# Performance work log

Measured on AMD Instinct MI355X. Metric: run time of the kernel, lower is better.

The kernel has to match this reference:

```python
import jax, jax.numpy as jnp
import numpy as np
from jax import lax

VOCAB, EMB, HID, SEQ, BATCH = 50000, 512, 256, 64, 128


def _lstm_dir(x, Wih, Whh, bih, bhh):
    # x: (L,B,E); Wih: (4H,E); Whh: (4H,H); torch gate order i,f,g,o
    B = x.shape[1]
    H = Whh.shape[1]
    xg = jnp.einsum('lbe,ge->lbg', x, Wih) + (bih + bhh)  # precompute input contribution

    def step(carry, g_in):
        h, c = carry
        g = g_in + h @ Whh.T
        i, f, gg, o = jnp.split(g, 4, axis=-1)
        c = jax.nn.sigmoid(f) * c + jax.nn.sigmoid(i) * jnp.tanh(gg)
        h = jax.nn.sigmoid(o) * jnp.tanh(c)
        return (h, c), h

    z = jnp.zeros((B, H), x.dtype)
    _, hs = lax.scan(step, (z, z), xg)
    return hs  # (L,B,H)


def _bilstm(x, Wih_f, Whh_f, bih_f, bhh_f, Wih_b, Whh_b, bih_b, bhh_b):
    hf = _lstm_dir(x, Wih_f, Whh_f, bih_f, bhh_f)
    hb = _lstm_dir(x[::-1], Wih_b, Whh_b, bih_b, bhh_b)[::-1]
    return jnp.concatenate([hf, hb], axis=-1)  # (L,B,2H)


def _forward(tokens1, tokens2, emb, Wih_f, Whh_f, bih_f, bhh_f, Wih_b, Whh_b, bih_b, bhh_b):
    L, B = tokens1.shape
    w = (Wih_f, Whh_f, bih_f, bhh_f, Wih_b, Whh_b, bih_b, bhh_b)
    # original applies self.lstm_1 to BOTH sentences (lstm_2 unused)
    o1 = _bilstm(emb[tokens1], *w)  # (L,B,D)
    o2 = _bilstm(emb[tokens2], *w)
    D = o1.shape[-1]
    mp1 = o1.max(axis=0)  # adaptive_max_pool1d over time -> (B,D)
    # torch .view on contiguous (L,B,D): raw reshape, replicated faithfully
    att = jnp.einsum('bd,bdl->bl', mp1, o2.reshape(B, D, L))
    att_sm = jax.nn.softmax(att, axis=1)  # per-row softmax over L
    new_pool = jnp.einsum('bl,bld->bd', att_sm, o2.reshape(B, L, D))
    # commonWords: d[i] = LAST index j in sen1 with sen1[j]==sen2[i], else -1
    s1, s2 = tokens1.T, tokens2.T  # (B,L)
    match = s2[:, :, None] == s1[:, None, :]  # (B,L2,L1)
    d = jnp.max(jnp.where(match, jnp.arange(L)[None, None, :], -1), axis=2)  # (B,L)
    mask = (d > 1) & (s2 > 0)  # note strict > 1 as in original
    pos = jnp.clip(d, 0, L - 1)
    o1b = jnp.transpose(o1, (1, 0, 2))  # (B,L,D)
    gath1 = jnp.take_along_axis(o1b, pos[:, :, None], axis=1)  # outputs_1[d[i], b]
    neg = jnp.finfo(o1.dtype).min
    has = jnp.any(mask, axis=1)[:, None]
    e1h = jnp.where(has, jnp.max(jnp.where(mask[:, :, None], gath1, neg), axis=1), 0.0)
    o2b = jnp.transpose(o2, (1, 0, 2))
    e2h = jnp.where(has, jnp.max(jnp.where(mask[:, :, None], o2b, neg), axis=1), 0.0)
    sim = jnp.exp(-jnp.sum(jnp.abs(mp1 - new_pool), axis=1))
    return sim, e1h, e2h


def setup_inputs() -> dict:
    key = jax.random.key(0)
    ks = jax.random.split(key, 8)
    H4 = 4 * HID

    def w(k, shape, fan):
        return (jax.random.normal(k, shape, jnp.float32) / np.float32(np.sqrt(fan))).astype(jnp.float32)

    return {
        'tokens1': jax.random.randint(ks[0], (SEQ, BATCH), 0, VOCAB),
        'tokens2': jax.random.randint(ks[1], (SEQ, BATCH), 0, VOCAB),
        'emb': jax.random.normal(ks[2], (VOCAB, EMB), jnp.float32) * 0.1,
        'Wih_f': w(ks[3], (H4, EMB), EMB),
        'Whh_f': w(ks[4], (H4, HID), HID),
        'bih_f': jnp.full((H4,), 0.01, jnp.float32),
        'bhh_f': jnp.full((H4,), 0.01, jnp.float32),
        'Wih_b': w(ks[5], (H4, EMB), EMB),
        'Whh_b': w(ks[6], (H4, HID), HID),
        'bih_b': jnp.full((H4,), 0.01, jnp.float32),
        'bhh_b': jnp.full((H4,), 0.01, jnp.float32),
    }


def reference(tokens1, tokens2, emb, Wih_f, Whh_f, bih_f, bhh_f, Wih_b, Whh_b, bih_b, bhh_b):
    return _forward(tokens1, tokens2, emb, Wih_f, Whh_f, bih_f, bhh_f, Wih_b, Whh_b, bih_b, bhh_b)
```

## Files before the change

kernel.cpp:

```cpp
#include <hip/hip_runtime.h>
#include <hip/hip_bf16.h>
#include <math.h>

#define L_SEQ 64
#define NB    128
#define EMBD  512
#define HID   256
#define G4    1024
#define NCOL  2048
#define DDIM  512
#define MS    (L_SEQ*NB)
#define MTOT  (2*MS)

typedef __bf16 bf16_t;
typedef bf16_t bf16x4 __attribute__((ext_vector_type(4)));
typedef bf16_t bf16x8 __attribute__((ext_vector_type(8)));
typedef float  floatx4 __attribute__((ext_vector_type(4)));
typedef float  floatx8 __attribute__((ext_vector_type(8)));

__device__ __forceinline__ bf16x8 cvt_bf16x8(floatx8 v) {
    bf16x8 r;
    r[0]=(bf16_t)v[0]; r[1]=(bf16_t)v[1]; r[2]=(bf16_t)v[2]; r[3]=(bf16_t)v[3];
    r[4]=(bf16_t)v[4]; r[5]=(bf16_t)v[5]; r[6]=(bf16_t)v[6]; r[7]=(bf16_t)v[7];
    return r;
}

__device__ __forceinline__ void gload_lds16(const bf16_t* g, bf16_t* l) {
    __builtin_amdgcn_global_load_lds(
        (const __attribute__((address_space(1))) unsigned int*)(g),
        (__attribute__((address_space(3))) unsigned int*)(l), 16, 0, 0);
}

__device__ __forceinline__ float fsigmoid(float x) {
    return __builtin_amdgcn_rcpf(1.0f + __expf(-x));
}
__device__ __forceinline__ float ftanh(float x) {
    return 1.0f - 2.0f * __builtin_amdgcn_rcpf(__expf(2.0f*x) + 1.0f);
}

#define LDS_BARRIER() asm volatile("s_waitcnt lgkmcnt(0)\n\ts_barrier" ::: "memory")

__global__ __launch_bounds__(256) void k_pack_a(const int* __restrict__ t1,
                                                const int* __restrict__ t2,
                                                const float* __restrict__ emb,
                                                bf16_t* __restrict__ A)
{
    int gid = blockIdx.x*256 + threadIdx.x;
    int row = gid >> 6;
    int k8  = (gid & 63) * 8;
    int tok = (row < MS) ? t1[row] : t2[row - MS];
    floatx8 v = *(const floatx8*)(emb + (size_t)tok*EMBD + k8);
    *(bf16x8*)(A + (size_t)row*EMBD + k8) = cvt_bf16x8(v);
}

__global__ __launch_bounds__(256) void k_pack_b(const float* __restrict__ wih_f,
                                                const float* __restrict__ wih_b,
                                                bf16_t* __restrict__ B)
{
    int gid = blockIdx.x*256 + threadIdx.x;
    int n   = gid >> 6;
    int k8  = (gid & 63) * 8;
    const float* src = (n >= 1024) ? (wih_b + (size_t)(n-1024)*EMBD)
                                   : (wih_f + (size_t)n*EMBD);
    *(bf16x8*)(B + (size_t)n*EMBD + k8) = cvt_bf16x8(*(const floatx8*)(src + k8));
}

__global__ __launch_bounds__(256) void k_pack_whh(const float* __restrict__ whh_f,
                                                  const float* __restrict__ whh_b,
                                                  bf16_t* __restrict__ whhB)
{
    int gid = blockIdx.x*256 + threadIdx.x;
    int r2  = gid >> 5;
    int k8  = (gid & 31) * 8;
    const float* src = (r2 >= 1024) ? (whh_b + (size_t)(r2-1024)*HID)
                                    : (whh_f + (size_t)r2*HID);
    *(bf16x8*)(whhB + (size_t)r2*HID + k8) = cvt_bf16x8(*(const floatx8*)(src + k8));
}

__global__ __launch_bounds__(256) void k_pack_bias(const float* __restrict__ bih_f,
                                                   const float* __restrict__ bhh_f,
                                                   const float* __restrict__ bih_b,
                                                   const float* __restrict__ bhh_b,
                                                   float* __restrict__ bias)
{
    int n = blockIdx.x*256 + threadIdx.x;
    bias[n] = (n >= 1024) ? (bih_b[n-1024] + bhh_b[n-1024])
                          : (bih_f[n] + bhh_f[n]);
}

__global__ __launch_bounds__(256) void xg_gemm4(const bf16_t* __restrict__ A,
                                                const bf16_t* __restrict__ B,
                                                const float* __restrict__ bias,
                                                bf16_t* __restrict__ xgT)
{
    __shared__ bf16_t As[128*32];
    __shared__ bf16_t Bs[128*32];
    const int tid  = threadIdx.x;
    const int wid  = tid >> 6;
    const int lane = tid & 63;
    const int l15  = lane & 15;
    const int quad = lane >> 4;
    const int m0   = blockIdx.y * 128;
    const int n0   = blockIdx.x * 128;
    const int mw   = (wid & 1) * 64;
    const int nw   = (wid >> 1) * 64;

    float biasv[4];
#pragma unroll
    for (int ni = 0; ni < 4; ++ni) biasv[ni] = bias[n0 + nw + ni*16 + l15];

    const int srow = tid >> 2;
    const int sk8  = (tid & 3) * 8;

    floatx4 acc[4][4] = {};
    for (int kk = 0; kk < EMBD; kk += 32) {
#pragma unroll
        for (int inst = 0; inst < 2; ++inst) {
            gload_lds16(A + (size_t)(m0 + inst*64 + srow)*EMBD + kk + sk8,
                        As + inst*2048 + wid*512);
            gload_lds16(B + (size_t)(n0 + inst*64 + srow)*EMBD + kk + sk8,
                        Bs + inst*2048 + wid*512);
        }
        __syncthreads();
        bf16x8 a[4], b[4];
#pragma unroll
        for (int mi = 0; mi < 4; ++mi)
            a[mi] = *(const bf16x8*)(As + (mw + mi*16 + l15)*32 + quad*8);
#pragma unroll
        for (int ni = 0; ni < 4; ++ni)
            b[ni] = *(const bf16x8*)(Bs + (nw + ni*16 + l15)*32 + quad*8);
#pragma unroll
        for (int mi = 0; mi < 4; ++mi)
#pragma unroll
            for (int ni = 0; ni < 4; ++ni)
                acc[mi][ni] = __builtin_amdgcn_mfma_f32_16x16x32_bf16(
                                  a[mi], b[ni], acc[mi][ni], 0, 0, 0);
        __syncthreads();
    }

    const int sent = blockIdx.y >> 6;
    const int l    = blockIdx.y & 63;
    const int dir  = n0 >> 10;
    const int s2   = sent*2 + dir;
#pragma unroll
    for (int mi = 0; mi < 4; ++mi)
#pragma unroll
        for (int ni = 0; ni < 4; ++ni) {
            int gcol = (n0 & 1023) + nw + ni*16 + l15;
            int b    = mw + mi*16 + quad*4;
            int ch   = b >> 4;
            int bi   = b & 15;
            bf16x4 v;
#pragma unroll
            for (int r = 0; r < 4; ++r) v[r] = (bf16_t)(acc[mi][ni][r] + biasv[ni]);
            *(bf16x4*)(xgT + ((size_t)((s2*8 + ch)*64 + l)*1024 + gcol)*16 + bi) = v;
        }
}

__global__
__attribute__((amdgpu_flat_work_group_size(1024, 1024), amdgpu_waves_per_eu(4, 4)))
void lstm_scan8(
    const bf16_t* __restrict__ whhB,
    const bf16_t* __restrict__ xgT,
    float* __restrict__ o1, float* __restrict__ o2)
{
    extern __shared__ char smem[];
    bf16_t* hb = (bf16_t*)smem;
    bf16_t* BL = (bf16_t*)(smem + 16384);

    const int tid  = threadIdx.x;
    const int wv   = tid >> 6;
    const int lane = tid & 63;
    const int l15  = lane & 15;
    const int quad = lane >> 4;
    const int s2   = blockIdx.y;
    const int sent = s2 >> 1;
    const int dr   = s2 & 1;
    const int chunk= blockIdx.x;
    const int b0   = chunk * 16;
    float* o = sent ? o2 : o1;
    const bf16_t* bb = whhB + (size_t)dr * (1024*HID);


#pragma unroll
    for (int g = 0; g < 4; ++g) {
        const int col = g*256 + wv*16 + l15;
#pragma unroll
        for (int ksl = 0; ksl < 2; ++ksl)
            gload_lds16(bb + (size_t)col*HID + (4+ksl)*32 + quad*8,
                        BL + (size_t)((wv*4 + g)*2 + ksl)*512);
    }

    bf16x8 bwc[4][4];
#pragma unroll
    for (int g = 0; g < 4; ++g) {
        const bf16_t* cp = bb + (size_t)(g*256 + wv*16 + l15)*HID + quad*8;
#pragma unroll
        for (int ks = 0; ks < 4; ++ks)
            bwc[g][ks] = *(const volatile bf16x8*)(cp + ks*32);
    }

    for (int i = tid; i < 4096; i += 1024) hb[i] = (bf16_t)0.0f;
    __syncthreads();

    float cst[4] = {};
    int pp = 0;

    for (int t = 0; t < L_SEQ; ++t) {
        const int lt = dr ? (L_SEQ-1-t) : t;
        asm volatile("" ::: "memory");

        bf16x4 xvc[4];
        {
            const bf16_t* xp = xgT + (size_t)((s2*8 + chunk)*64 + lt)*16384;
#pragma unroll
            for (int g = 0; g < 4; ++g)
                xvc[g] = *(const bf16x4*)(xp + (size_t)(g*256 + wv*16 + l15)*16
                                          + quad*4);
        }

        floatx4 acc[4] = {};
        if (t > 0) {
            bf16x8 sb[4];
#pragma unroll
            for (int g = 0; g < 4; ++g) {
                const bf16_t* cp = bb + (size_t)(g*256 + wv*16 + l15)*HID;
                sb[g] = *(const bf16x8*)(cp + 6*32 + quad*8);
            }

            const bf16_t* fr = hb + pp*4096;
#pragma unroll
            for (int ks = 0; ks < 4; ++ks) {
                bf16x8 af = *(const bf16x8*)(fr + ((ks*4 + quad)*16 + l15)*8);
#pragma unroll
                for (int g = 0; g < 4; ++g)
                    acc[g] = __builtin_amdgcn_mfma_f32_16x16x32_bf16(
                                 af, bwc[g][ks], acc[g], 0, 0, 0);
            }
            {
                bf16x8 af6 = *(const bf16x8*)(fr + ((6*4 + quad)*16 + l15)*8);
#pragma unroll
                for (int g = 0; g < 4; ++g)
                    acc[g] = __builtin_amdgcn_mfma_f32_16x16x32_bf16(
                                 af6, sb[g], acc[g], 0, 0, 0);
            }
#pragma unroll
            for (int g = 0; g < 4; ++g) {
                const bf16_t* cp = bb + (size_t)(g*256 + wv*16 + l15)*HID;
                sb[g] = *(const bf16x8*)(cp + 7*32 + quad*8);
            }
#pragma unroll
            for (int ksl = 0; ksl < 2; ++ksl) {
                bf16x8 af = *(const bf16x8*)(fr + (((4+ksl)*4 + quad)*16 + l15)*8);
#pragma unroll
                for (int g = 0; g < 4; ++g) {
                    bf16x8 bl = *(const bf16x8*)(BL + (size_t)((wv*4 + g)*2 + ksl)*512
                                                 + lane*8);
                    acc[g] = __builtin_amdgcn_mfma_f32_16x16x32_bf16(
                                 af, bl, acc[g], 0, 0, 0);
                }
            }
            {
                bf16x8 af7 = *(const bf16x8*)(fr + ((7*4 + quad)*16 + l15)*8);
#pragma unroll
                for (int g = 0; g < 4; ++g)
                    acc[g] = __builtin_amdgcn_mfma_f32_16x16x32_bf16(
                                 af7, sb[g], acc[g], 0, 0, 0);
            }
        }

        bf16_t* fw = hb + (pp^1)*4096;
        const int j = wv*16 + l15;
        float* orow = o + (size_t)(lt*NB + b0)*DDIM + dr*HID + j;
#pragma unroll
        for (int r = 0; r < 4; ++r) {
            const int m = quad*4 + r;
            float gi = acc[0][r] + (float)xvc[0][r];
            float gf = acc[1][r] + (float)xvc[1][r];
            float gg = acc[2][r] + (float)xvc[2][r];
            float go = acc[3][r] + (float)xvc[3][r];
            float cv = fsigmoid(gf)*cst[r] + fsigmoid(gi)*ftanh(gg);
            cst[r] = cv;
            float hv = fsigmoid(go)*ftanh(cv);
            orow[(size_t)m*DDIM] = hv;
            fw[((j >> 3)*16 + m)*8 + (j & 7)] = (bf16_t)hv;
        }
        LDS_BARRIER();
        pp ^= 1;
    }
}

__global__ __launch_bounds__(256) void k_mp1(const float* __restrict__ o1,
                                             float* __restrict__ mp1)
{
    int gid = blockIdx.x*256 + threadIdx.x;
    float m = -3.402823466e+38f;
    for (int l = 0; l < L_SEQ; ++l)
        m = fmaxf(m, o1[(size_t)l*(NB*DDIM) + gid]);
    mp1[gid] = m;
}

__global__ __launch_bounds__(256) void k_att(const float* __restrict__ o2,
                                             const float* __restrict__ mp1,
                                             float* __restrict__ sim)
{
    const int b   = blockIdx.x;
    const int tid = threadIdx.x;
    const int l   = tid & 63;
    const int cp  = tid >> 6;
    __shared__ float spart[256];
    __shared__ float satt[64], sexp[64], ssm[64];
    __shared__ float red[256];

    const float* o2b = o2  + (size_t)b*32768;
    const float* mpb = mp1 + b*DDIM;

    float p = 0.0f;
    for (int d = cp*128; d < cp*128 + 128; ++d)
        p += mpb[d] * o2b[d*64 + l];
    spart[tid] = p;
    __syncthreads();
    if (tid < 64)
        satt[tid] = spart[tid] + spart[tid+64] + spart[tid+128] + spart[tid+192];
    __syncthreads();
    if (tid < 64) {
        float mx = satt[0];
        for (int i = 1; i < 64; ++i) mx = fmaxf(mx, satt[i]);
        sexp[tid] = expf(satt[tid] - mx);
    }
    __syncthreads();
    if (tid < 64) {
        float s = 0.0f;
        for (int i = 0; i < 64; ++i) s += sexp[i];
        ssm[tid] = sexp[tid] / s;
    }
    __syncthreads();

    float np0 = 0.0f, np1 = 0.0f;
    for (int l2 = 0; l2 < 64; ++l2) {
        float smv = ssm[l2];
        np0 += smv * o2b[l2*DDIM + tid];
        np1 += smv * o2b[l2*DDIM + tid + 256];
    }
    float diff = fabsf(mpb[tid] - np0) + fabsf(mpb[tid+256] - np1);
    red[tid] = diff;
    __syncthreads();
    for (int s = 128; s > 0; s >>= 1) {
        if (tid < s) red[tid] += red[tid + s];
        __syncthreads();
    }
    if (tid == 0) sim[b] = expf(-red[0]);
}

__global__ __launch_bounds__(256) void k_common(
    const int*   __restrict__ t1, const int* __restrict__ t2,
    const float* __restrict__ o1, const float* __restrict__ o2,
    float* __restrict__ e1h, float* __restrict__ e2h)
{
    const int b   = blockIdx.x;
    const int tid = threadIdx.x;
    __shared__ int ss1[64];
    __shared__ int smask[64];
    __shared__ int spos[64];
    __shared__ int sany;
    if (tid == 0) sany = 0;
    if (tid < 64) ss1[tid] = t1[tid*NB + b];
    __syncthreads();
    if (tid < 64) {
        int s2 = t2[tid*NB + b];
        int dmax = -1;
        for (int j = 0; j < 64; ++j)
            if (ss1[j] == s2) dmax = j;
        int mk = (dmax > 1) && (s2 > 0);
        smask[tid] = mk;
        spos[tid]  = dmax < 0 ? 0 : dmax;
        if (mk) sany = 1;
    }
    __syncthreads();
    int has = sany;
#pragma unroll
    for (int half = 0; half < 2; ++half) {
        int dd = tid + half*256;
        float m1 = -3.402823466e+38f, m2 = -3.402823466e+38f;
        for (int i = 0; i < 64; ++i) {
            if (smask[i]) {
                m1 = fmaxf(m1, o1[(size_t)spos[i]*(NB*DDIM) + b*DDIM + dd]);
                m2 = fmaxf(m2, o2[(size_t)i      *(NB*DDIM) + b*DDIM + dd]);
            }
        }
        e1h[b*DDIM + dd] = has ? m1 : 0.0f;
        e2h[b*DDIM + dd] = has ? m2 : 0.0f;
    }
}

extern "C" void kernel_launch(void* const* d_in, const int* in_sizes, int n_in,
                              void* d_out, int out_size, void* d_ws, size_t ws_size,
                              hipStream_t stream)
{
    (void)in_sizes; (void)n_in; (void)out_size; (void)ws_size;
    const int*   t1    = (const int*)d_in[0];
    const int*   t2    = (const int*)d_in[1];
    const float* emb   = (const float*)d_in[2];
    const float* wih_f = (const float*)d_in[3];
    const float* whh_f = (const float*)d_in[4];
    const float* bih_f = (const float*)d_in[5];
    const float* bhh_f = (const float*)d_in[6];
    const float* wih_b = (const float*)d_in[7];
    const float* whh_b = (const float*)d_in[8];
    const float* bih_b = (const float*)d_in[9];
    const float* bhh_b = (const float*)d_in[10];
    float* out = (float*)d_out;

    char* ws = (char*)d_ws;
    size_t off = 0;
    auto carve = [&](size_t bytes) -> void* {
        void* p = ws + off;
        off = (off + bytes + 255) & ~(size_t)255;
        return p;
    };
    float*  o1    = (float*)carve(sizeof(float)*(size_t)L_SEQ*NB*DDIM);
    float*  o2    = (float*)carve(sizeof(float)*(size_t)L_SEQ*NB*DDIM);
    bf16_t* whhB  = (bf16_t*)carve(sizeof(bf16_t)*2*1024*HID);
    bf16_t* Bw    = (bf16_t*)carve(sizeof(bf16_t)*(size_t)NCOL*EMBD);
    float*  bias  = (float*)carve(sizeof(float)*NCOL);
    float*  mp1   = (float*)carve(sizeof(float)*NB*DDIM);
    bf16_t* xgT   = (bf16_t*)carve(sizeof(bf16_t)*(size_t)MTOT*NCOL);
    bf16_t* A     = (bf16_t*)o1;

    hipFuncSetAttribute((const void*)lstm_scan8,
                        hipFuncAttributeMaxDynamicSharedMemorySize, 147456);

    hipLaunchKernelGGL(k_pack_a,    dim3(4096), dim3(256), 0, stream, t1, t2, emb, A);
    hipLaunchKernelGGL(k_pack_b,    dim3(512),  dim3(256), 0, stream, wih_f, wih_b, Bw);
    hipLaunchKernelGGL(k_pack_whh,  dim3(256),  dim3(256), 0, stream, whh_f, whh_b, whhB);
    hipLaunchKernelGGL(k_pack_bias, dim3(8),    dim3(256), 0, stream,
                       bih_f, bhh_f, bih_b, bhh_b, bias);

    hipLaunchKernelGGL(xg_gemm4, dim3(16, 128), dim3(256), 0, stream, A, Bw, bias, xgT);

    hipLaunchKernelGGL(lstm_scan8, dim3(8, 4), dim3(1024), 147456, stream,
                       whhB, xgT, o1, o2);

    hipLaunchKernelGGL(k_mp1,    dim3(256), dim3(256), 0, stream, o1, mp1);
    hipLaunchKernelGGL(k_att,    dim3(128), dim3(256), 0, stream, o2, mp1, out);
    hipLaunchKernelGGL(k_common, dim3(128), dim3(256), 0, stream,
                       t1, t2, o1, o2, out + NB, out + NB + NB*DDIM);
}
```

Baseline: 618.4 us.

## Split each LSTM scan block across two workgroups exchanging hidden state via global flags

The recurrent scan now uses two 512-thread workgroups per (sentence, direction, batch chunk) instead of one 1024-thread block. Each half owns 128 hidden units, keeps its full Whh slice in registers (no LDS or global reloads of weight k-slices), and swaps its half of h with the partner each step through a global double buffer guarded by acquire/release flag spins. This doubles the CUs working on the serial recurrence and removes the weight-streaming traffic. In exchange it adds cross-CU synchronisation latency on every timestep and depends on both partner workgroups being co-resident.

```diff
diff --git a/kernel.cpp b/kernel.cpp
--- a/kernel.cpp
+++ b/kernel.cpp
@@ -81,11 +81,13 @@
                                                    const float* __restrict__ bhh_f,
                                                    const float* __restrict__ bih_b,
                                                    const float* __restrict__ bhh_b,
-                                                   float* __restrict__ bias)
+                                                   float* __restrict__ bias,
+                                                   unsigned* __restrict__ flags)
 {
     int n = blockIdx.x*256 + threadIdx.x;
     bias[n] = (n >= 1024) ? (bih_b[n-1024] + bhh_b[n-1024])
                           : (bih_f[n] + bhh_f[n]);
+    if (blockIdx.x == 0 && threadIdx.x < 64) flags[threadIdx.x] = 0u;
 }
 
 __global__ __launch_bounds__(256) void xg_gemm4(const bf16_t* __restrict__ A,
@@ -158,50 +160,48 @@
 }
 
 __global__
-__attribute__((amdgpu_flat_work_group_size(1024, 1024), amdgpu_waves_per_eu(4, 4)))
-void lstm_scan8(
+__attribute__((amdgpu_flat_work_group_size(512, 512), amdgpu_waves_per_eu(2, 2)))
+void lstm_scan9(
     const bf16_t* __restrict__ whhB,
     const bf16_t* __restrict__ xgT,
-    float* __restrict__ o1, float* __restrict__ o2)
-{
-    extern __shared__ char smem[];
-    bf16_t* hb = (bf16_t*)smem;
-    bf16_t* BL = (bf16_t*)(smem + 16384);
+    float* __restrict__ o1, float* __restrict__ o2,
+    bf16_t* __restrict__ hx,
+    unsigned* __restrict__ flags)
+{
+    __shared__ bf16_t hb[2*2048];
 
     const int tid  = threadIdx.x;
     const int wv   = tid >> 6;
     const int lane = tid & 63;
     const int l15  = lane & 15;
     const int quad = lane >> 4;
+    const int chunk= blockIdx.x;
     const int s2   = blockIdx.y;
+    const int half = blockIdx.z;
     const int sent = s2 >> 1;
     const int dr   = s2 & 1;
-    const int chunk= blockIdx.x;
     const int b0   = chunk * 16;
     float* o = sent ? o2 : o1;
     const bf16_t* bb = whhB + (size_t)dr * (1024*HID);
 
-
+    const int fi = (s2*8 + chunk)*2 + half;
+    bf16_t*  myBuf  = hx + (size_t)fi*4096;
+    const bf16_t* pBuf = hx + (size_t)(fi^1)*4096;
+    unsigned* myFlag = flags + fi;
+    const unsigned* pFlag = flags + (fi^1);
+
+    const int jl  = wv*16 + l15;
+    const int ownKs = half * 4;
+    const int parKs = 4 - ownKs;
+
+    bf16x8 bwc[4][8];
 #pragma unroll
     for (int g = 0; g < 4; ++g) {
-        const int col = g*256 + wv*16 + l15;
-#pragma unroll
-        for (int ksl = 0; ksl < 2; ++ksl)
-            gload_lds16(bb + (size_t)col*HID + (4+ksl)*32 + quad*8,
-                        BL + (size_t)((wv*4 + g)*2 + ksl)*512);
-    }
-
-    bf16x8 bwc[4][4];
-#pragma unroll
-    for (int g = 0; g < 4; ++g) {
-        const bf16_t* cp = bb + (size_t)(g*256 + wv*16 + l15)*HID + quad*8;
-#pragma unroll
-        for (int ks = 0; ks < 4; ++ks)
+        const bf16_t* cp = bb + (size_t)(g*256 + half*128 + jl)*HID + quad*8;
+#pragma unroll
+        for (int ks = 0; ks < 8; ++ks)
             bwc[g][ks] = *(const volatile bf16x8*)(cp + ks*32);
     }
-
-    for (int i = tid; i < 4096; i += 1024) hb[i] = (bf16_t)0.0f;
-    __syncthreads();
 
     float cst[4] = {};
     int pp = 0;
@@ -210,68 +210,50 @@
         const int lt = dr ? (L_SEQ-1-t) : t;
         asm volatile("" ::: "memory");
 
+        bf16x8 pa[4];
+        if (t > 0) {
+            while (__hip_atomic_load(pFlag, __ATOMIC_ACQUIRE,
+                                     __HIP_MEMORY_SCOPE_AGENT) < (unsigned)t)
+                __builtin_amdgcn_s_sleep(2);
+            const bf16_t* pb = pBuf + ((t-1)&1)*2048;
+#pragma unroll
+            for (int ksl = 0; ksl < 4; ++ksl)
+                pa[ksl] = *(const bf16x8*)(pb + ((ksl*4 + quad)*16 + l15)*8);
+        }
+
         bf16x4 xvc[4];
         {
             const bf16_t* xp = xgT + (size_t)((s2*8 + chunk)*64 + lt)*16384;
 #pragma unroll
             for (int g = 0; g < 4; ++g)
-                xvc[g] = *(const bf16x4*)(xp + (size_t)(g*256 + wv*16 + l15)*16
+                xvc[g] = *(const bf16x4*)(xp + (size_t)(g*256 + half*128 + jl)*16
                                           + quad*4);
         }
 
         floatx4 acc[4] = {};
         if (t > 0) {
-            bf16x8 sb[4];
-#pragma unroll
-            for (int g = 0; g < 4; ++g) {
-                const bf16_t* cp = bb + (size_t)(g*256 + wv*16 + l15)*HID;
-                sb[g] = *(const bf16x8*)(cp + 6*32 + quad*8);
-            }
-
-            const bf16_t* fr = hb + pp*4096;
-#pragma unroll
-            for (int ks = 0; ks < 4; ++ks) {
-                bf16x8 af = *(const bf16x8*)(fr + ((ks*4 + quad)*16 + l15)*8);
+            const bf16_t* fr = hb + pp*2048;
+#pragma unroll
+            for (int ksl = 0; ksl < 4; ++ksl) {
+                bf16x8 af = *(const bf16x8*)(fr + ((ksl*4 + quad)*16 + l15)*8);
 #pragma unroll
                 for (int g = 0; g < 4; ++g)
                     acc[g] = __builtin_amdgcn_mfma_f32_16x16x32_bf16(
-                                 af, bwc[g][ks], acc[g], 0, 0, 0);
+                                 af, bwc[g][ownKs + ksl], acc[g], 0, 0, 0);
             }
-            {
-                bf16x8 af6 = *(const bf16x8*)(fr + ((6*4 + quad)*16 + l15)*8);
+#pragma unroll
+            for (int ksl = 0; ksl < 4; ++ksl) {
 #pragma unroll
                 for (int g = 0; g < 4; ++g)
                     acc[g] = __builtin_amdgcn_mfma_f32_16x16x32_bf16(
-                                 af6, sb[g], acc[g], 0, 0, 0);
+                                 pa[ksl], bwc[g][parKs + ksl], acc[g], 0, 0, 0);
             }
-#pragma unroll
-            for (int g = 0; g < 4; ++g) {
-                const bf16_t* cp = bb + (size_t)(g*256 + wv*16 + l15)*HID;
-                sb[g] = *(const bf16x8*)(cp + 7*32 + quad*8);
-            }
-#pragma unroll
-            for (int ksl = 0; ksl < 2; ++ksl) {
-                bf16x8 af = *(const bf16x8*)(fr + (((4+ksl)*4 + quad)*16 + l15)*8);
-#pragma unroll
-                for (int g = 0; g < 4; ++g) {
-                    bf16x8 bl = *(const bf16x8*)(BL + (size_t)((wv*4 + g)*2 + ksl)*512
-                                                 + lane*8);
-                    acc[g] = __builtin_amdgcn_mfma_f32_16x16x32_bf16(
-                                 af, bl, acc[g], 0, 0, 0);
-                }
-            }
-            {
-                bf16x8 af7 = *(const bf16x8*)(fr + ((7*4 + quad)*16 + l15)*8);
-#pragma unroll
-                for (int g = 0; g < 4; ++g)
-                    acc[g] = __builtin_amdgcn_mfma_f32_16x16x32_bf16(
-                                 af7, sb[g], acc[g], 0, 0, 0);
-            }
-        }
-
-        bf16_t* fw = hb + (pp^1)*4096;
-        const int j = wv*16 + l15;
-        float* orow = o + (size_t)(lt*NB + b0)*DDIM + dr*HID + j;
+        }
+
+        bf16_t* fw = hb + (pp^1)*2048;
+        bf16_t* gw = myBuf + (t&1)*2048;
+        float* orow = o + (size_t)(lt*NB + b0)*DDIM + dr*HID + half*128 + jl;
+        float hvf[4];
 #pragma unroll
         for (int r = 0; r < 4; ++r) {
             const int m = quad*4 + r;
@@ -282,9 +264,21 @@
             float cv = fsigmoid(gf)*cst[r] + fsigmoid(gi)*ftanh(gg);
             cst[r] = cv;
             float hv = fsigmoid(go)*ftanh(cv);
-            orow[(size_t)m*DDIM] = hv;
-            fw[((j >> 3)*16 + m)*8 + (j & 7)] = (bf16_t)hv;
-        }
+            hvf[r] = hv;
+            bf16_t hvb = (bf16_t)hv;
+            const int idx = ((jl >> 3)*16 + m)*8 + (jl & 7);
+            fw[idx] = hvb;
+            gw[idx] = hvb;
+        }
+
+        __builtin_amdgcn_fence(__ATOMIC_RELEASE, "agent");
+        __hip_atomic_store(myFlag, (unsigned)(t+1), __ATOMIC_RELAXED,
+                           __HIP_MEMORY_SCOPE_AGENT);
+
+#pragma unroll
+        for (int r = 0; r < 4; ++r)
+            orow[(size_t)(quad*4 + r)*DDIM] = hvf[r];
+
         LDS_BARRIER();
         pp ^= 1;
     }
@@ -418,28 +412,27 @@
         off = (off + bytes + 255) & ~(size_t)255;
         return p;
     };
-    float*  o1    = (float*)carve(sizeof(float)*(size_t)L_SEQ*NB*DDIM);
-    float*  o2    = (float*)carve(sizeof(float)*(size_t)L_SEQ*NB*DDIM);
-    bf16_t* whhB  = (bf16_t*)carve(sizeof(bf16_t)*2*1024*HID);
-    bf16_t* Bw    = (bf16_t*)carve(sizeof(bf16_t)*(size_t)NCOL*EMBD);
-    float*  bias  = (float*)carve(sizeof(float)*NCOL);
-    float*  mp1   = (float*)carve(sizeof(float)*NB*DDIM);
-    bf16_t* xgT   = (bf16_t*)carve(sizeof(bf16_t)*(size_t)MTOT*NCOL);
-    bf16_t* A     = (bf16_t*)o1;
-
-    hipFuncSetAttribute((const void*)lstm_scan8,
-                        hipFuncAttributeMaxDynamicSharedMemorySize, 147456);
+    float*    o1    = (float*)carve(sizeof(float)*(size_t)L_SEQ*NB*DDIM);
+    float*    o2    = (float*)carve(sizeof(float)*(size_t)L_SEQ*NB*DDIM);
+    bf16_t*   whhB  = (bf16_t*)carve(sizeof(bf16_t)*2*1024*HID);
+    bf16_t*   Bw    = (bf16_t*)carve(sizeof(bf16_t)*(size_t)NCOL*EMBD);
+    float*    bias  = (float*)carve(sizeof(float)*NCOL);
+    float*    mp1   = (float*)carve(sizeof(float)*NB*DDIM);
+    bf16_t*   hx    = (bf16_t*)carve(sizeof(bf16_t)*64*4096);
+    unsigned* flags = (unsigned*)carve(sizeof(unsigned)*64);
+    bf16_t*   xgT   = (bf16_t*)carve(sizeof(bf16_t)*(size_t)MTOT*NCOL);
+    bf16_t*   A     = (bf16_t*)o1;
 
     hipLaunchKernelGGL(k_pack_a,    dim3(4096), dim3(256), 0, stream, t1, t2, emb, A);
     hipLaunchKernelGGL(k_pack_b,    dim3(512),  dim3(256), 0, stream, wih_f, wih_b, Bw);
     hipLaunchKernelGGL(k_pack_whh,  dim3(256),  dim3(256), 0, stream, whh_f, whh_b, whhB);
     hipLaunchKernelGGL(k_pack_bias, dim3(8),    dim3(256), 0, stream,
-                       bih_f, bhh_f, bih_b, bhh_b, bias);
+                       bih_f, bhh_f, bih_b, bhh_b, bias, flags);
 
     hipLaunchKernelGGL(xg_gemm4, dim3(16, 128), dim3(256), 0, stream, A, Bw, bias, xgT);
 
-    hipLaunchKernelGGL(lstm_scan8, dim3(8, 4), dim3(1024), 147456, stream,
-                       whhB, xgT, o1, o2);
+    hipLaunchKernelGGL(lstm_scan9, dim3(8, 4, 2), dim3(512), 0, stream,
+                       whhB, xgT, o1, o2, hx, flags);
 
     hipLaunchKernelGGL(k_mp1,    dim3(256), dim3(256), 0, stream, o1, mp1);
     hipLaunchKernelGGL(k_att,    dim3(128), dim3(256), 0, stream, o2, mp1, out);
```

New measurement: 1.813 ms. 2.93x slower.
